# Optimization experiments

Measured on AMD Instinct MI355X. Metric: run time of the kernel, lower is better.

Reference implementation:

```python
import jax, jax.numpy as jnp
import numpy as np

NH = 32
LN_EPS = 1e-5

def _mlp2(x, w1, b1, w2, b2):
    # Linear -> ReLU -> Linear (torch convention: y = x @ W^T + b)
    return jnp.maximum(x @ w1.T + b1, 0.0) @ w2.T + b2

def _layernorm(x, g, b):
    m = x.mean(-1, keepdims=True)
    v = jnp.mean((x - m) ** 2, axis=-1, keepdims=True)
    return (x - m) / jnp.sqrt(v + LN_EPS) * g + b

def _pos_enc(pos):
    # P[..., 2i] = sin(pos/(i+1)*pi), P[..., 2i+1] = cos(pos/(i+1)*pi)
    i = jnp.arange(NH // 2, dtype=pos.dtype)
    ang = pos[..., None] * (jnp.pi / (i + 1.0))  # [B, L, NH/2]
    return jnp.stack([jnp.sin(ang), jnp.cos(ang)], axis=-1).reshape(pos.shape[0], pos.shape[1], NH)

def _forward(x0, x1, pos0, pos1, xcT,
             e0w1, e0b1, e0w2, e0b2,
             e1w1, e1b1, e1w2, e1b2,
             ecw1, ecb1, ecw2, ecb2,
             wq, wk, wv, wo,
             ln1g, ln1b, ln2g, ln2b,
             f1w1, f1b1, f1w2, f1b2,
             f2w1, f2b1, f2w2, f2b2,
             l0, l1):
    # InputFeature
    e0 = _mlp2(x0, e0w1, e0b1, e0w2, e0b2) + _pos_enc(pos0)      # [B, l0, 32]
    e1 = _mlp2(x1, e1w1, e1b1, e1w2, e1b2) + _pos_enc(pos1)      # [B, l1, 32]
    ec = _mlp2(xcT, ecw1, ecb1, ecw2, ecb2)                      # [B, 32]
    xIn = jnp.concatenate([e0, e1, ec[:, None, :]], axis=1)      # [B, L, 32], L = l0+l1+1
    # AttentionLayer: attention over the feature axis (faithful to bmm(q^T, k))
    q = xIn @ wq.T; k = xIn @ wk.T; v = xIn @ wv.T               # [B, L, 32]
    L = xIn.shape[1]
    score = jnp.einsum('blh,blg->bhg', q, k) / jnp.sqrt(jnp.asarray(L, xIn.dtype))  # [B, 32, 32]
    att = jax.nn.softmax(score, axis=-1)
    a = jnp.einsum('bhg,blg->blh', att, v) @ wo.T                # [B, L, 32]
    # addnorm1 (dropout in eval = identity) + ffn1 + addnorm2 + ffn2
    h1 = _layernorm(a + xIn, ln1g, ln1b)
    h2 = _mlp2(h1, f1w1, f1b1, f1w2, f1b2)
    h3 = _layernorm(h2 + xIn, ln2g, ln2b)
    y = _mlp2(h3, f2w1, f2b1, f2w2, f2b2)[..., 0]                # [B, L]
    # segment-mean pooling: sum of per-segment means (last segment = xc token)
    return y[:, :l0].mean(-1) + y[:, l0:l0 + l1].mean(-1) + y[:, l0 + l1:].mean(-1)

def setup_inputs() -> dict:
    key = jax.random.key(0)
    ks = iter(jax.random.split(key, 48))
    B, L0, L1, N0, N1, NXC = 2048, 365, 366, 8, 16, 32
    lin = lambda o, i: jax.random.normal(next(ks), (o, i), jnp.float32) * np.float32(1.0 / np.sqrt(i))
    d = {}
    d['x0'] = jax.random.normal(next(ks), (B, L0, N0), jnp.float32)
    d['x1'] = jax.random.normal(next(ks), (B, L1, N1), jnp.float32)
    d['pos0'] = jax.random.uniform(next(ks), (B, L0), jnp.float32) * 365.0
    d['pos1'] = jax.random.uniform(next(ks), (B, L1), jnp.float32) * 365.0
    d['xcT'] = jax.random.normal(next(ks), (B, NXC), jnp.float32)
    d['e0w1'] = lin(NH, N0); d['e0b1'] = jnp.zeros((NH,), jnp.float32)
    d['e0w2'] = lin(NH, NH); d['e0b2'] = jnp.zeros((NH,), jnp.float32)
    d['e1w1'] = lin(NH, N1); d['e1b1'] = jnp.zeros((NH,), jnp.float32)
    d['e1w2'] = lin(NH, NH); d['e1b2'] = jnp.zeros((NH,), jnp.float32)
    d['ecw1'] = lin(NH, NXC); d['ecb1'] = jnp.zeros((NH,), jnp.float32)
    d['ecw2'] = lin(NH, NH); d['ecb2'] = jnp.zeros((NH,), jnp.float32)
    d['wq'] = lin(NH, NH); d['wk'] = lin(NH, NH); d['wv'] = lin(NH, NH); d['wo'] = lin(NH, NH)
    d['ln1g'] = jnp.ones((NH,), jnp.float32); d['ln1b'] = jnp.zeros((NH,), jnp.float32)
    d['ln2g'] = jnp.ones((NH,), jnp.float32); d['ln2b'] = jnp.zeros((NH,), jnp.float32)
    d['f1w1'] = lin(NH, NH); d['f1b1'] = jnp.zeros((NH,), jnp.float32)
    d['f1w2'] = lin(NH, NH); d['f1b2'] = jnp.zeros((NH,), jnp.float32)
    d['f2w1'] = lin(NH, NH); d['f2b1'] = jnp.zeros((NH,), jnp.float32)
    d['f2w2'] = lin(1, NH); d['f2b2'] = jnp.zeros((1,), jnp.float32)
    d['l0'] = L0; d['l1'] = L1
    return d

def reference(x0, x1, pos0, pos1, xcT,
              e0w1, e0b1, e0w2, e0b2, e1w1, e1b1, e1w2, e1b2,
              ecw1, ecb1, ecw2, ecb2, wq, wk, wv, wo,
              ln1g, ln1b, ln2g, ln2b,
              f1w1, f1b1, f1w2, f1b2, f2w1, f2b1, f2w2, f2b2,
              l0, l1):
    return _forward(x0, x1, pos0, pos1, xcT,
                    e0w1, e0b1, e0w2, e0b2, e1w1, e1b1, e1w2, e1b2,
                    ecw1, ecb1, ecw2, ecb2, wq, wk, wv, wo,
                    ln1g, ln1b, ln2g, ln2b,
                    f1w1, f1b1, f1w2, f1b2, f2w1, f2b1, f2w2, f2b2,
                    l0, l1)
```

## Files before the change

kernel.cpp:

```cpp
#include <hip/hip_runtime.h>
#include <math.h>

#define L0T 365
#define L1T 366
#define LT  732
#define NTILE 46
#define NSEG 23
#define NW   4
#define NTHR 256

typedef short svec8 __attribute__((ext_vector_type(8)));
typedef float fvec4 __attribute__((ext_vector_type(4)));
typedef float fvec16 __attribute__((ext_vector_type(16)));
typedef unsigned uvec4 __attribute__((ext_vector_type(4)));

__device__ __forceinline__ unsigned short f2bf(float f) {
    unsigned u = __float_as_uint(f);
    u = (u + 0x7fffu + ((u >> 16) & 1u)) >> 16;
    return (unsigned short)u;
}
__device__ __forceinline__ float bf2f(unsigned short s) {
    return __uint_as_float(((unsigned)s) << 16);
}
__device__ __forceinline__ unsigned pk2(float a, float b) {
    return (unsigned)f2bf(a) | ((unsigned)f2bf(b) << 16);
}
__device__ __forceinline__ unsigned cvtpk(float a, float b) {
    unsigned r;
    asm("v_cvt_pk_bf16_f32 %0, %1, %2" : "=v"(r) : "v"(a), "v"(b));
    return r;
}
__device__ __forceinline__ float pgetv(uvec4 p, int j) {
    unsigned u = p[j >> 1];
    return bf2f((unsigned short)((j & 1) ? (u >> 16) : (u & 0xffffu)));
}
__device__ __forceinline__ svec8 pack8(float4 a, float4 c) {
    uvec4 u;
    u[0] = cvtpk(a.x, a.y); u[1] = cvtpk(a.z, a.w);
    u[2] = cvtpk(c.x, c.y); u[3] = cvtpk(c.z, c.w);
    return __builtin_bit_cast(svec8, u);
}
__device__ __forceinline__ void fastsc(float rev, float& s, float& c) {
    float fr;
    asm("v_fract_f32 %0, %1" : "=v"(fr) : "v"(rev));
    asm("v_sin_f32 %0, %1"   : "=v"(s)  : "v"(fr));
    asm("v_cos_f32 %0, %1"   : "=v"(c)  : "v"(fr));
}

__device__ __forceinline__ void embed_pass(
    const unsigned short* __restrict__ T1,
    const unsigned short* __restrict__ T2,
    const float* __restrict__ Bh, const float* __restrict__ Bx,
    svec8 bx, int ln, int Q, float* __restrict__ out)
{
    svec8 w1f0 = *(const svec8*)&T1[ln * 8];
    svec8 w1f1 = *(const svec8*)&T1[512 + ln * 8];
    const fvec4* bh = (const fvec4*)&Bh[Q * 8];
    fvec4 d0 = __builtin_amdgcn_mfma_f32_16x16x32_bf16(w1f0, bx, bh[0], 0, 0, 0);
    fvec4 d1 = __builtin_amdgcn_mfma_f32_16x16x32_bf16(w1f1, bx, bh[1], 0, 0, 0);
    uvec4 hu;
    hu[0] = cvtpk(fmaxf(d0[0], 0.f), fmaxf(d0[1], 0.f));
    hu[1] = cvtpk(fmaxf(d0[2], 0.f), fmaxf(d0[3], 0.f));
    hu[2] = cvtpk(fmaxf(d1[0], 0.f), fmaxf(d1[1], 0.f));
    hu[3] = cvtpk(fmaxf(d1[2], 0.f), fmaxf(d1[3], 0.f));
    svec8 hf = __builtin_bit_cast(svec8, hu);
    svec8 w2f0 = *(const svec8*)&T2[ln * 8];
    svec8 w2f1 = *(const svec8*)&T2[512 + ln * 8];
    const fvec4* bb = (const fvec4*)&Bx[Q * 8];
    fvec4 g0 = __builtin_amdgcn_mfma_f32_16x16x32_bf16(w2f0, hf, bb[0], 0, 0, 0);
    fvec4 g1 = __builtin_amdgcn_mfma_f32_16x16x32_bf16(w2f1, hf, bb[1], 0, 0, 0);
    out[0] = g0[0]; out[1] = g0[1]; out[2] = g0[2]; out[3] = g0[3];
    out[4] = g1[0]; out[5] = g1[1]; out[6] = g1[2]; out[7] = g1[3];
}

__device__ __forceinline__ void load_tile(
    int t, int b, int tk, int Q,
    const float* __restrict__ x0, const float* __restrict__ x1,
    const float* __restrict__ pos0, const float* __restrict__ pos1,
    svec8& bx, float& pv, int& seg, int& tl)
{
    seg = (t >= NSEG) ? 1 : 0;
    tl  = (seg ? (t - NSEG) : t) * 16 + tk;
    const int lim = seg ? L1T : L0T;
    const bool tvalid = tl < lim;
    #pragma unroll
    for (int j = 0; j < 8; j++) bx[j] = 0;
    const bool ld = tvalid && (seg ? (Q < 2) : (Q == 0));
    if (ld) {
        const float4* px = seg
            ? (const float4*)(x1 + ((size_t)b * L1T + tl) * 16 + Q * 8)
            : (const float4*)(x0 + ((size_t)b * L0T + tl) * 8);
        bx = pack8(px[0], px[1]);
    }
    pv = 0.f;
    if (tvalid) pv = seg ? pos1[(size_t)b * L1T + tl] : pos0[(size_t)b * L0T + tl];
}

__device__ __forceinline__ void finish_xv(
    int seg, int tl, int Q, const float* __restrict__ e, float pv, float4 pwr,
    const float* __restrict__ ECV, float* __restrict__ xv)
{
    const int lim = seg ? L1T : L0T;
    const bool tvalid = tl < lim;
    const bool isxc = seg && (tl == L1T);
    const float pwa[4] = {pwr.x, pwr.y, pwr.z, pwr.w};
    #pragma unroll
    for (int j = 0; j < 8; j += 2) {
        float s, c; fastsc(pv * pwa[j >> 1], s, c);
        float a0 = e[j] + s, a1 = e[j + 1] + c;
        xv[j]     = tvalid ? a0 : (isxc ? ECV[Q * 8 + j]     : 0.f);
        xv[j + 1] = tvalid ? a1 : (isxc ? ECV[Q * 8 + j + 1] : 0.f);
    }
}

__global__ __launch_bounds__(NTHR, 4) void fused_kernel(
    const float* __restrict__ x0,  const float* __restrict__ x1,
    const float* __restrict__ pos0,const float* __restrict__ pos1,
    const float* __restrict__ xcT,
    const float* __restrict__ e0w1,const float* __restrict__ e0b1,
    const float* __restrict__ e0w2,const float* __restrict__ e0b2,
    const float* __restrict__ e1w1,const float* __restrict__ e1b1,
    const float* __restrict__ e1w2,const float* __restrict__ e1b2,
    const float* __restrict__ ecw1,const float* __restrict__ ecb1,
    const float* __restrict__ ecw2,const float* __restrict__ ecb2,
    const float* __restrict__ wq,  const float* __restrict__ wk,
    const float* __restrict__ wv,  const float* __restrict__ wo,
    const float* __restrict__ ln1g,const float* __restrict__ ln1b,
    const float* __restrict__ ln2g,const float* __restrict__ ln2b,
    const float* __restrict__ f1w1,const float* __restrict__ f1b1,
    const float* __restrict__ f1w2,const float* __restrict__ f1b2,
    const float* __restrict__ f2w1,const float* __restrict__ f2b1,
    const float* __restrict__ f2w2,const float* __restrict__ f2b2,
    float* __restrict__ out)
{
    const int b   = blockIdx.x;
    const int tid = threadIdx.x;
    const int w   = tid >> 6;
    const int ln  = tid & 63;
    const int tk  = ln & 15;
    const int Q   = ln >> 4;
    const int Lr0 = ((tk >> 2) * 8) + (tk & 3);
    const int Lr1 = Lr0 + 4;

    __shared__ unsigned short TBL[4 * 1024] __attribute__((aligned(16)));
    __shared__ float BIA[128] __attribute__((aligned(16)));
    __shared__ unsigned PCK[128] __attribute__((aligned(16)));
    __shared__ float SCR[2048] __attribute__((aligned(16)));
    __shared__ unsigned short Wbb[1024] __attribute__((aligned(16)));
    __shared__ float ECV[32] __attribute__((aligned(16)));
    __shared__ float red[NW * 3];

    float* T1f  = SCR;
    float* CmT2 = SCR + 1024;

    float4 pwr;
    pwr.x = 0.5f / (float)(Q * 4 + 1);
    pwr.y = 0.5f / (float)(Q * 4 + 2);
    pwr.z = 0.5f / (float)(Q * 4 + 3);
    pwr.w = 0.5f / (float)(Q * 4 + 4);

    for (int idx = tid; idx < 1024; idx += NTHR) {
        int f = idx >> 9, lane = (idx >> 3) & 63, j = idx & 7;
        int tkk = lane & 15, QQ = lane >> 4;
        int Lr = ((tkk >> 2) * 8) + (tkk & 3) + f * 4;
        int col = QQ * 8 + j;
        TBL[idx]        = (col < 8)  ? f2bf(e0w1[Lr * 8  + col]) : (unsigned short)0;
        TBL[1024 + idx] = f2bf(e0w2[Lr * 32 + col]);
        TBL[2048 + idx] = (col < 16) ? f2bf(e1w1[Lr * 16 + col]) : (unsigned short)0;
        TBL[3072 + idx] = f2bf(e1w2[Lr * 32 + col]);
        CmT2[idx] = 0.f;
    }
    if (tid < 128) {
        int s = tid >> 5, i = tid & 31;
        float bv;
        if      (s == 0) bv = e0b1[i];
        else if (s == 1) bv = e0b2[i];
        else if (s == 2) bv = e1b1[i];
        else             bv = e1b2[i];
        BIA[tid] = bv;
    }
    if (tid < 128) {
        int t8 = tid >> 4, q = (tid >> 2) & 3, i = tid & 3, f = q * 8 + 2 * i;
        const float* sp;
        if      (t8 == 0) sp = ln1g;
        else if (t8 == 1) sp = ln1b;
        else if (t8 == 2) sp = ln2g;
        else if (t8 == 3) sp = ln2b;
        else if (t8 == 4) sp = f1b1;
        else if (t8 == 5) sp = f1b2;
        else if (t8 == 6) sp = f2b1;
        else              sp = f2w2;
        PCK[tid] = pk2(sp[f], sp[f + 1]);
    }
    float* ECH = T1f;
    if (tid >= 224) {
        int i = tid - 224;
        const float4* xr = (const float4*)(xcT + (size_t)b * 32);
        const float4* wr = (const float4*)&ecw1[i * 32];
        float a = ecb1[i];
        #pragma unroll
        for (int j4 = 0; j4 < 8; j4++) {
            float4 ww = wr[j4], xx = xr[j4];
            a = fmaf(ww.x, xx.x, a); a = fmaf(ww.y, xx.y, a);
            a = fmaf(ww.z, xx.z, a); a = fmaf(ww.w, xx.w, a);
        }
        ECH[i] = fmaxf(a, 0.f);
    }
    __syncthreads();
    if (tid >= 224) {
        int i = tid - 224;
        const float4* wr = (const float4*)&ecw2[i * 32];
        float a = ecb2[i];
        #pragma unroll
        for (int j4 = 0; j4 < 8; j4++) {
            float4 ww = wr[j4];
            a = fmaf(ww.x, ECH[j4 * 4 + 0], a); a = fmaf(ww.y, ECH[j4 * 4 + 1], a);
            a = fmaf(ww.z, ECH[j4 * 4 + 2], a); a = fmaf(ww.w, ECH[j4 * 4 + 3], a);
        }
        ECV[i] = a;
    }
    __syncthreads();

    {
        unsigned short* ST = (unsigned short*)T1f;
        const int feat = ln & 31, half = ln >> 5;
        fvec16 dG;
        #pragma unroll
        for (int i = 0; i < 16; i++) dG[i] = 0.f;

        auto embed_core = [&](int seg, svec8 bx, float* e) {
            const unsigned short* T = TBL + seg * 2048;
            const float* Bb = BIA + seg * 64;
            embed_pass(T, T + 1024, Bb, Bb + 32, bx, ln, Q, e);
        };
        auto gram_step = [&](const float* xv) {
            uvec4 pk;
            pk[0] = cvtpk(xv[0], xv[1]); pk[1] = cvtpk(xv[2], xv[3]);
            pk[2] = cvtpk(xv[4], xv[5]); pk[3] = cvtpk(xv[6], xv[7]);
            *(uvec4*)&ST[(w * 16 + tk) * 32 + Q * 8] = pk;
            svec8 af;
            #pragma unroll
            for (int j = 0; j < 8; j++)
                af[j] = (short)ST[w * 512 + (half * 8 + j) * 32 + feat];
            dG = __builtin_amdgcn_mfma_f32_32x32x16_bf16(af, af, dG, 0, 0, 0);
        };

        float xv[8];
        {
            svec8 bx; float pv; int sg, tl;
            load_tile(w, b, tk, Q, x0, x1, pos0, pos1, bx, pv, sg, tl);
            float e[8]; embed_core(sg, bx, e);
            finish_xv(sg, tl, Q, e, pv, pwr, ECV, xv);
        }
        for (int tn = w + NW; tn < NTILE; tn += NW) {
            svec8 bxN; float pvN; int sgN, tlN;
            load_tile(tn, b, tk, Q, x0, x1, pos0, pos1, bxN, pvN, sgN, tlN);
            float eN[8]; embed_core(sgN, bxN, eN);
            float xvN[8]; finish_xv(sgN, tlN, Q, eN, pvN, pwr, ECV, xvN);
            gram_step(xv);
            #pragma unroll
            for (int j = 0; j < 8; j++) xv[j] = xvN[j];
        }
        gram_step(xv);

        #pragma unroll
        for (int rg = 0; rg < 16; rg++) {
            int row = (rg & 3) + 8 * (rg >> 2) + 4 * half;
            atomicAdd(&CmT2[row * 32 + feat], dG[rg]);
        }
    }
    __syncthreads();

    for (int idx = tid; idx < 1024; idx += NTHR) {
        int i = idx >> 5, g = idx & 31;
        const float4* cr = (const float4*)&CmT2[i * 32];
        const float4* wr = (const float4*)&wk[g * 32];
        float a = 0.f;
        #pragma unroll
        for (int j4 = 0; j4 < 8; j4++) {
            float4 cc = cr[j4], ww = wr[j4];
            a = fmaf(cc.x, ww.x, a); a = fmaf(cc.y, ww.y, a);
            a = fmaf(cc.z, ww.z, a); a = fmaf(cc.w, ww.w, a);
        }
        T1f[idx] = a;
    }
    __syncthreads();
    const float rsL = rsqrtf((float)LT);
    for (int idx = tid; idx < 1024; idx += NTHR) {
        int h = idx >> 5, g = idx & 31;
        const float4* qr = (const float4*)&wq[h * 32];
        float a = 0.f;
        #pragma unroll
        for (int i4 = 0; i4 < 8; i4++) {
            float4 qq = qr[i4];
            a = fmaf(qq.x, T1f[(i4 * 4 + 0) * 32 + g], a);
            a = fmaf(qq.y, T1f[(i4 * 4 + 1) * 32 + g], a);
            a = fmaf(qq.z, T1f[(i4 * 4 + 2) * 32 + g], a);
            a = fmaf(qq.w, T1f[(i4 * 4 + 3) * 32 + g], a);
        }
        CmT2[idx] = a * rsL;
    }
    __syncthreads();
    {
        int r = tid >> 3, c0 = (tid & 7) * 4;
        float4 vv = *(const float4*)&CmT2[r * 32 + c0];
        float m = fmaxf(fmaxf(vv.x, vv.y), fmaxf(vv.z, vv.w));
        m = fmaxf(m, __shfl_xor(m, 1));
        m = fmaxf(m, __shfl_xor(m, 2));
        m = fmaxf(m, __shfl_xor(m, 4));
        float ex = __expf(vv.x - m), ey = __expf(vv.y - m);
        float ez = __expf(vv.z - m), ew = __expf(vv.w - m);
        float s = ex + ey + ez + ew;
        s += __shfl_xor(s, 1); s += __shfl_xor(s, 2); s += __shfl_xor(s, 4);
        float inv = 1.f / s;
        float4 o; o.x = ex * inv; o.y = ey * inv; o.z = ez * inv; o.w = ew * inv;
        *(float4*)&CmT2[r * 32 + c0] = o;
    }
    __syncthreads();
    for (int idx = tid; idx < 1024; idx += NTHR) {
        int h = idx >> 5, j = idx & 31;
        const float4* pr = (const float4*)&CmT2[h * 32];
        float a = 0.f;
        #pragma unroll
        for (int g4 = 0; g4 < 8; g4++) {
            float4 pp = pr[g4];
            a = fmaf(pp.x, wv[(g4 * 4 + 0) * 32 + j], a);
            a = fmaf(pp.y, wv[(g4 * 4 + 1) * 32 + j], a);
            a = fmaf(pp.z, wv[(g4 * 4 + 2) * 32 + j], a);
            a = fmaf(pp.w, wv[(g4 * 4 + 3) * 32 + j], a);
        }
        T1f[idx] = a;
    }
    __syncthreads();
    for (int idx = tid; idx < 1024; idx += NTHR) {
        int o = idx >> 5, j = idx & 31;
        const float4* orow = (const float4*)&wo[o * 32];
        float a = 0.f;
        #pragma unroll
        for (int h4 = 0; h4 < 8; h4++) {
            float4 oo = orow[h4];
            a = fmaf(oo.x, T1f[(h4 * 4 + 0) * 32 + j], a);
            a = fmaf(oo.y, T1f[(h4 * 4 + 1) * 32 + j], a);
            a = fmaf(oo.z, T1f[(h4 * 4 + 2) * 32 + j], a);
            a = fmaf(oo.w, T1f[(h4 * 4 + 3) * 32 + j], a);
        }
        Wbb[idx] = f2bf(a + (o == j ? 1.f : 0.f));
    }
    __syncthreads();

    svec8 wbf0 = *(const svec8*)&Wbb[Lr0 * 32 + Q * 8];
    svec8 wbf1 = *(const svec8*)&Wbb[Lr1 * 32 + Q * 8];
    svec8 a1f0, a1f1, a2f0, a2f1, a3f0, a3f1;
    #pragma unroll
    for (int j = 0; j < 8; j++) {
        a1f0[j] = (short)f2bf(f1w1[Lr0 * 32 + Q * 8 + j]);
        a1f1[j] = (short)f2bf(f1w1[Lr1 * 32 + Q * 8 + j]);
        a2f0[j] = (short)f2bf(f1w2[Lr0 * 32 + Q * 8 + j]);
        a2f1[j] = (short)f2bf(f1w2[Lr1 * 32 + Q * 8 + j]);
        a3f0[j] = (short)f2bf(f2w1[Lr0 * 32 + Q * 8 + j]);
        a3f1[j] = (short)f2bf(f2w1[Lr1 * 32 + Q * 8 + j]);
    }
    const float ybias = f2b2[0];
    const fvec4 zc = {0.f, 0.f, 0.f, 0.f};
    const uvec4* P4 = (const uvec4*)PCK;

    float s0 = 0.f, s1 = 0.f, s2 = 0.f;
    {
        auto embed_core = [&](int seg, svec8 bx, float* e) {
            const unsigned short* T = TBL + seg * 2048;
            const float* Bb = BIA + seg * 64;
            embed_pass(T, T + 1024, Bb, Bb + 32, bx, ln, Q, e);
        };
        auto pipe_rest = [&](const float* xv) -> float {
            uvec4 pkx;
            pkx[0] = cvtpk(xv[0], xv[1]); pkx[1] = cvtpk(xv[2], xv[3]);
            pkx[2] = cvtpk(xv[4], xv[5]); pkx[3] = cvtpk(xv[6], xv[7]);
            svec8 bx = __builtin_bit_cast(svec8, pkx);
            fvec4 d0 = __builtin_amdgcn_mfma_f32_16x16x32_bf16(wbf0, bx, zc, 0, 0, 0);
            fvec4 d1 = __builtin_amdgcn_mfma_f32_16x16x32_bf16(wbf1, bx, zc, 0, 0, 0);
            float v[8];
            #pragma unroll
            for (int j = 0; j < 4; j++) { v[j] = d0[j]; v[4 + j] = d1[j]; }
            float S = 0.f, Sq = 0.f;
            #pragma unroll
            for (int j = 0; j < 8; j++) { S += v[j]; Sq = fmaf(v[j], v[j], Sq); }
            S  += __shfl_xor(S, 16);  Sq += __shfl_xor(Sq, 16);
            S  += __shfl_xor(S, 32);  Sq += __shfl_xor(Sq, 32);
            float mean = S * (1.f / 32.f);
            float var = fmaxf(Sq * (1.f / 32.f) - mean * mean, 0.f);
            float rs = rsqrtf(var + 1e-5f);
            uvec4 pg1 = P4[Q], pb1 = P4[4 + Q];
            float n[8];
            #pragma unroll
            for (int j = 0; j < 8; j++)
                n[j] = (v[j] - mean) * rs * pgetv(pg1, j) + pgetv(pb1, j);
            uvec4 tu;
            tu[0] = cvtpk(n[0], n[1]); tu[1] = cvtpk(n[2], n[3]);
            tu[2] = cvtpk(n[4], n[5]); tu[3] = cvtpk(n[6], n[7]);
            svec8 tf = __builtin_bit_cast(svec8, tu);
            fvec4 u0 = __builtin_amdgcn_mfma_f32_16x16x32_bf16(a1f0, tf, zc, 0, 0, 0);
            fvec4 u1 = __builtin_amdgcn_mfma_f32_16x16x32_bf16(a1f1, tf, zc, 0, 0, 0);
            uvec4 pc1 = P4[16 + Q];
            uvec4 uu;
            uu[0] = cvtpk(fmaxf(u0[0] + pgetv(pc1, 0), 0.f), fmaxf(u0[1] + pgetv(pc1, 1), 0.f));
            uu[1] = cvtpk(fmaxf(u0[2] + pgetv(pc1, 2), 0.f), fmaxf(u0[3] + pgetv(pc1, 3), 0.f));
            uu[2] = cvtpk(fmaxf(u1[0] + pgetv(pc1, 4), 0.f), fmaxf(u1[1] + pgetv(pc1, 5), 0.f));
            uu[3] = cvtpk(fmaxf(u1[2] + pgetv(pc1, 6), 0.f), fmaxf(u1[3] + pgetv(pc1, 7), 0.f));
            svec8 uf = __builtin_bit_cast(svec8, uu);
            fvec4 g0 = __builtin_amdgcn_mfma_f32_16x16x32_bf16(a2f0, uf, zc, 0, 0, 0);
            fvec4 g1 = __builtin_amdgcn_mfma_f32_16x16x32_bf16(a2f1, uf, zc, 0, 0, 0);
            uvec4 pc2 = P4[20 + Q];
            #pragma unroll
            for (int j = 0; j < 8; j++)
                v[j] = (j < 4 ? g0[j] : g1[j - 4]) + pgetv(pc2, j) + xv[j];
            float S2 = 0.f, Sq2 = 0.f;
            #pragma unroll
            for (int j = 0; j < 8; j++) { S2 += v[j]; Sq2 = fmaf(v[j], v[j], Sq2); }
            S2  += __shfl_xor(S2, 16);  Sq2 += __shfl_xor(Sq2, 16);
            S2  += __shfl_xor(S2, 32);  Sq2 += __shfl_xor(Sq2, 32);
            float mean2 = S2 * (1.f / 32.f);
            float var2 = fmaxf(Sq2 * (1.f / 32.f) - mean2 * mean2, 0.f);
            float rs2 = rsqrtf(var2 + 1e-5f);
            uvec4 pg2 = P4[8 + Q], pb2 = P4[12 + Q];
            float n2[8];
            #pragma unroll
            for (int j = 0; j < 8; j++)
                n2[j] = (v[j] - mean2) * rs2 * pgetv(pg2, j) + pgetv(pb2, j);
            uvec4 t2u;
            t2u[0] = cvtpk(n2[0], n2[1]); t2u[1] = cvtpk(n2[2], n2[3]);
            t2u[2] = cvtpk(n2[4], n2[5]); t2u[3] = cvtpk(n2[6], n2[7]);
            svec8 t2 = __builtin_bit_cast(svec8, t2u);
            fvec4 q0 = __builtin_amdgcn_mfma_f32_16x16x32_bf16(a3f0, t2, zc, 0, 0, 0);
            fvec4 q1 = __builtin_amdgcn_mfma_f32_16x16x32_bf16(a3f1, t2, zc, 0, 0, 0);
            uvec4 pc3 = P4[24 + Q], pw2 = P4[28 + Q];
            float yp = 0.f;
            #pragma unroll
            for (int j = 0; j < 8; j++) {
                float e = (j < 4 ? q0[j] : q1[j - 4]) + pgetv(pc3, j);
                yp = fmaf(pgetv(pw2, j), fmaxf(e, 0.f), yp);
            }
            yp += __shfl_xor(yp, 16); yp += __shfl_xor(yp, 32);
            return yp;
        };
        auto accum_y = [&](int seg, int tl, float yp) {
            if (Q == 0) {
                float yv = yp + ybias;
                if (seg == 0) { if (tl < L0T) s0 += yv; }
                else {
                    if (tl < L1T)       s1 += yv;
                    else if (tl == L1T) s2 += yv;
                }
            }
        };

        float xv[8]; int sg, tl;
        {
            svec8 bx; float pv;
            load_tile(w, b, tk, Q, x0, x1, pos0, pos1, bx, pv, sg, tl);
            float e[8]; embed_core(sg, bx, e);
            finish_xv(sg, tl, Q, e, pv, pwr, ECV, xv);
        }
        for (int tn = w + NW; tn < NTILE; tn += NW) {
            svec8 bxN; float pvN; int sgN, tlN;
            load_tile(tn, b, tk, Q, x0, x1, pos0, pos1, bxN, pvN, sgN, tlN);
            float eN[8]; embed_core(sgN, bxN, eN);
            float xvN[8]; finish_xv(sgN, tlN, Q, eN, pvN, pwr, ECV, xvN);
            float yp = pipe_rest(xv);
            accum_y(sg, tl, yp);
            #pragma unroll
            for (int j = 0; j < 8; j++) xv[j] = xvN[j];
            sg = sgN; tl = tlN;
        }
        accum_y(sg, tl, pipe_rest(xv));
    }

    s0 += __shfl_xor(s0, 1); s0 += __shfl_xor(s0, 2);
    s0 += __shfl_xor(s0, 4); s0 += __shfl_xor(s0, 8);
    s1 += __shfl_xor(s1, 1); s1 += __shfl_xor(s1, 2);
    s1 += __shfl_xor(s1, 4); s1 += __shfl_xor(s1, 8);
    s2 += __shfl_xor(s2, 1); s2 += __shfl_xor(s2, 2);
    s2 += __shfl_xor(s2, 4); s2 += __shfl_xor(s2, 8);
    if (ln == 0) { red[w * 3] = s0; red[w * 3 + 1] = s1; red[w * 3 + 2] = s2; }
    __syncthreads();
    if (tid == 0) {
        float a0 = 0.f, a1 = 0.f, a2 = 0.f;
        #pragma unroll
        for (int k = 0; k < NW; k++) {
            a0 += red[k * 3]; a1 += red[k * 3 + 1]; a2 += red[k * 3 + 2];
        }
        out[b] = a0 / (float)L0T + a1 / (float)L1T + a2;
    }
}

extern "C" void kernel_launch(void* const* d_in, const int* in_sizes, int n_in,
                              void* d_out, int out_size, void* d_ws, size_t ws_size,
                              hipStream_t stream)
{
    const float* x0   = (const float*)d_in[0];
    const float* x1   = (const float*)d_in[1];
    const float* pos0 = (const float*)d_in[2];
    const float* pos1 = (const float*)d_in[3];
    const float* xcT  = (const float*)d_in[4];
    const float* e0w1 = (const float*)d_in[5];
    const float* e0b1 = (const float*)d_in[6];
    const float* e0w2 = (const float*)d_in[7];
    const float* e0b2 = (const float*)d_in[8];
    const float* e1w1 = (const float*)d_in[9];
    const float* e1b1 = (const float*)d_in[10];
    const float* e1w2 = (const float*)d_in[11];
    const float* e1b2 = (const float*)d_in[12];
    const float* ecw1 = (const float*)d_in[13];
    const float* ecb1 = (const float*)d_in[14];
    const float* ecw2 = (const float*)d_in[15];
    const float* ecb2 = (const float*)d_in[16];
    const float* wq   = (const float*)d_in[17];
    const float* wk   = (const float*)d_in[18];
    const float* wv   = (const float*)d_in[19];
    const float* wo   = (const float*)d_in[20];
    const float* ln1g = (const float*)d_in[21];
    const float* ln1b = (const float*)d_in[22];
    const float* ln2g = (const float*)d_in[23];
    const float* ln2b = (const float*)d_in[24];
    const float* f1w1 = (const float*)d_in[25];
    const float* f1b1 = (const float*)d_in[26];
    const float* f1w2 = (const float*)d_in[27];
    const float* f1b2 = (const float*)d_in[28];
    const float* f2w1 = (const float*)d_in[29];
    const float* f2b1 = (const float*)d_in[30];
    const float* f2w2 = (const float*)d_in[31];
    const float* f2b2 = (const float*)d_in[32];
    float* out = (float*)d_out;

    const int B = in_sizes[0] / (L0T * 8);

    hipLaunchKernelGGL(fused_kernel, dim3(B), dim3(NTHR), 0, stream,
                       x0, x1, pos0, pos1, xcT,
                       e0w1, e0b1, e0w2, e0b2, e1w1, e1b1, e1w2, e1b2,
                       ecw1, ecb1, ecw2, ecb2, wq, wk, wv, wo,
                       ln1g, ln1b, ln2g, ln2b,
                       f1w1, f1b1, f1w2, f1b2, f2w1, f2b1, f2w2, f2b2,
                       out);
}
```

Baseline: 333.9 us.

## Cache bf16 embedded tiles in registers instead of recomputing embeddings in second pass

The first pass (Gram accumulation) now keeps each tile's packed bf16 embedding in a register array of 12 slots. The second pass reuses these values instead of reloading inputs and recomputing the embedding MLP and positional encoding. This removes a full second round of global loads and embedding arithmetic, at the cost of 48 extra VGPRs live across the attention-weight computation. The residual also now uses the bf16-rounded xIn instead of the fp32 value, and sched_barriers constrain scheduling in the first loop.

```diff
diff --git a/kernel.cpp b/kernel.cpp
--- a/kernel.cpp
+++ b/kernel.cpp
@@ -8,6 +8,7 @@
 #define NSEG 23
 #define NW   4
 #define NTHR 256
+#define NSLOT 12
 
 typedef short svec8 __attribute__((ext_vector_type(8)));
 typedef float fvec4 __attribute__((ext_vector_type(4)));
@@ -221,6 +222,8 @@
     }
     __syncthreads();
 
+    uvec4 xs[NSLOT];
+
     {
         unsigned short* ST = (unsigned short*)T1f;
         const int feat = ln & 31, half = ln >> 5;
@@ -228,41 +231,34 @@
         #pragma unroll
         for (int i = 0; i < 16; i++) dG[i] = 0.f;
 
-        auto embed_core = [&](int seg, svec8 bx, float* e) {
-            const unsigned short* T = TBL + seg * 2048;
-            const float* Bb = BIA + seg * 64;
-            embed_pass(T, T + 1024, Bb, Bb + 32, bx, ln, Q, e);
-        };
-        auto gram_step = [&](const float* xv) {
-            uvec4 pk;
-            pk[0] = cvtpk(xv[0], xv[1]); pk[1] = cvtpk(xv[2], xv[3]);
-            pk[2] = cvtpk(xv[4], xv[5]); pk[3] = cvtpk(xv[6], xv[7]);
-            *(uvec4*)&ST[(w * 16 + tk) * 32 + Q * 8] = pk;
-            svec8 af;
-            #pragma unroll
-            for (int j = 0; j < 8; j++)
-                af[j] = (short)ST[w * 512 + (half * 8 + j) * 32 + feat];
-            dG = __builtin_amdgcn_mfma_f32_32x32x16_bf16(af, af, dG, 0, 0, 0);
-        };
-
-        float xv[8];
-        {
-            svec8 bx; float pv; int sg, tl;
-            load_tile(w, b, tk, Q, x0, x1, pos0, pos1, bx, pv, sg, tl);
-            float e[8]; embed_core(sg, bx, e);
-            finish_xv(sg, tl, Q, e, pv, pwr, ECV, xv);
-        }
-        for (int tn = w + NW; tn < NTILE; tn += NW) {
-            svec8 bxN; float pvN; int sgN, tlN;
-            load_tile(tn, b, tk, Q, x0, x1, pos0, pos1, bxN, pvN, sgN, tlN);
-            float eN[8]; embed_core(sgN, bxN, eN);
-            float xvN[8]; finish_xv(sgN, tlN, Q, eN, pvN, pwr, ECV, xvN);
-            gram_step(xv);
-            #pragma unroll
-            for (int j = 0; j < 8; j++) xv[j] = xvN[j];
-        }
-        gram_step(xv);
-
+        #pragma unroll
+        for (int s = 0; s < NSLOT; s++) {
+            const int t = s * NW + w;
+            if (t < NTILE) {
+                svec8 bx; float pv; int sg, tl;
+                load_tile(t, b, tk, Q, x0, x1, pos0, pos1, bx, pv, sg, tl);
+                float e[8];
+                {
+                    const unsigned short* T = TBL + sg * 2048;
+                    const float* Bb = BIA + sg * 64;
+                    embed_pass(T, T + 1024, Bb, Bb + 32, bx, ln, Q, e);
+                }
+                float xv[8]; finish_xv(sg, tl, Q, e, pv, pwr, ECV, xv);
+                uvec4 pk;
+                pk[0] = cvtpk(xv[0], xv[1]); pk[1] = cvtpk(xv[2], xv[3]);
+                pk[2] = cvtpk(xv[4], xv[5]); pk[3] = cvtpk(xv[6], xv[7]);
+                xs[s] = pk;
+                __builtin_amdgcn_sched_barrier(0);
+                *(uvec4*)&ST[(w * 16 + tk) * 32 + Q * 8] = pk;
+                __builtin_amdgcn_sched_barrier(0);
+                svec8 af;
+                #pragma unroll
+                for (int j = 0; j < 8; j++)
+                    af[j] = (short)ST[w * 512 + (half * 8 + j) * 32 + feat];
+                __builtin_amdgcn_sched_barrier(0);
+                dG = __builtin_amdgcn_mfma_f32_32x32x16_bf16(af, af, dG, 0, 0, 0);
+            }
+        }
         #pragma unroll
         for (int rg = 0; rg < 16; rg++) {
             int row = (rg & 3) + 8 * (rg >> 2) + 4 * half;
@@ -365,17 +361,16 @@
     const uvec4* P4 = (const uvec4*)PCK;
 
     float s0 = 0.f, s1 = 0.f, s2 = 0.f;
-    {
-        auto embed_core = [&](int seg, svec8 bx, float* e) {
-            const unsigned short* T = TBL + seg * 2048;
-            const float* Bb = BIA + seg * 64;
-            embed_pass(T, T + 1024, Bb, Bb + 32, bx, ln, Q, e);
-        };
-        auto pipe_rest = [&](const float* xv) -> float {
-            uvec4 pkx;
-            pkx[0] = cvtpk(xv[0], xv[1]); pkx[1] = cvtpk(xv[2], xv[3]);
-            pkx[2] = cvtpk(xv[4], xv[5]); pkx[3] = cvtpk(xv[6], xv[7]);
-            svec8 bx = __builtin_bit_cast(svec8, pkx);
+    #pragma unroll
+    for (int s = 0; s < NSLOT; s++) {
+        const int t = s * NW + w;
+        if (t < NTILE) {
+            const uvec4 px = xs[s];
+            svec8 bx = __builtin_bit_cast(svec8, px);
+            float xf[8];
+            #pragma unroll
+            for (int j = 0; j < 8; j++) xf[j] = pgetv(px, j);
+
             fvec4 d0 = __builtin_amdgcn_mfma_f32_16x16x32_bf16(wbf0, bx, zc, 0, 0, 0);
             fvec4 d1 = __builtin_amdgcn_mfma_f32_16x16x32_bf16(wbf1, bx, zc, 0, 0, 0);
             float v[8];
@@ -412,7 +407,7 @@
             uvec4 pc2 = P4[20 + Q];
             #pragma unroll
             for (int j = 0; j < 8; j++)
-                v[j] = (j < 4 ? g0[j] : g1[j - 4]) + pgetv(pc2, j) + xv[j];
+                v[j] = (j < 4 ? g0[j] : g1[j - 4]) + pgetv(pc2, j) + xf[j];
             float S2 = 0.f, Sq2 = 0.f;
             #pragma unroll
             for (int j = 0; j < 8; j++) { S2 += v[j]; Sq2 = fmaf(v[j], v[j], Sq2); }
@@ -440,38 +435,17 @@
                 yp = fmaf(pgetv(pw2, j), fmaxf(e, 0.f), yp);
             }
             yp += __shfl_xor(yp, 16); yp += __shfl_xor(yp, 32);
-            return yp;
-        };
-        auto accum_y = [&](int seg, int tl, float yp) {
             if (Q == 0) {
+                const int sg = (t >= NSEG) ? 1 : 0;
+                const int tl = (sg ? (t - NSEG) : t) * 16 + tk;
                 float yv = yp + ybias;
-                if (seg == 0) { if (tl < L0T) s0 += yv; }
+                if (sg == 0) { if (tl < L0T) s0 += yv; }
                 else {
                     if (tl < L1T)       s1 += yv;
                     else if (tl == L1T) s2 += yv;
                 }
             }
-        };
-
-        float xv[8]; int sg, tl;
-        {
-            svec8 bx; float pv;
-            load_tile(w, b, tk, Q, x0, x1, pos0, pos1, bx, pv, sg, tl);
-            float e[8]; embed_core(sg, bx, e);
-            finish_xv(sg, tl, Q, e, pv, pwr, ECV, xv);
-        }
-        for (int tn = w + NW; tn < NTILE; tn += NW) {
-            svec8 bxN; float pvN; int sgN, tlN;
-            load_tile(tn, b, tk, Q, x0, x1, pos0, pos1, bxN, pvN, sgN, tlN);
-            float eN[8]; embed_core(sgN, bxN, eN);
-            float xvN[8]; finish_xv(sgN, tlN, Q, eN, pvN, pwr, ECV, xvN);
-            float yp = pipe_rest(xv);
-            accum_y(sg, tl, yp);
-            #pragma unroll
-            for (int j = 0; j < 8; j++) xv[j] = xvN[j];
-            sg = sgN; tl = tlN;
-        }
-        accum_y(sg, tl, pipe_rest(xv));
+        }
     }
 
     s0 += __shfl_xor(s0, 1); s0 += __shfl_xor(s0, 2);
```

Measured after the change: 327.2 us. -2.0%, faster.
